# Optimization experiments

Measured on AMD Instinct MI355X. Metric: run time of the kernel, lower is better.

Reference implementation:

```python
import jax, jax.numpy as jnp
import numpy as np

H = 2048      # num_hidden
B = 2048      # batch_size
T = 64        # seq_length
C = 10        # num_classes


def setup_inputs() -> dict:
    key = jax.random.key(0)
    k = jax.random.split(key, 4)
    bound = float(np.sqrt(1.0 / H))  # uniform(-bound, bound) init as in the torch module
    return {
        "x": jax.random.normal(k[0], (B, T), dtype=jnp.float32),
        "W_hx": jax.random.uniform(k[1], (H, 1), jnp.float32, -bound, bound),
        "W_hh": jax.random.uniform(k[2], (H, H), jnp.float32, -bound, bound),
        "W_hy": jax.random.uniform(k[3], (H, C), jnp.float32, -bound, bound),
        "b_h": jnp.zeros((H, 1), jnp.float32),
        "b_p": jnp.zeros((C, 1), jnp.float32),
    }


def reference(x, W_hx, W_hh, W_hy, b_h, b_p):
    # x: [B, T]; hidden state kept as [H, B] to match the torch layout.
    xT = x.T  # [T, B] so scan iterates over time

    def step(h, xt):
        # W_hx @ x_t  : [H,1] @ [1,B] -> [H,B]; W_hh @ h : [H,B]
        h = jnp.tanh(W_hx @ xt[None, :] + W_hh @ h + b_h)
        return h, None

    h0 = jnp.zeros((W_hh.shape[0], x.shape[0]), x.dtype)
    hT, _ = jax.lax.scan(step, h0, xT)
    out = W_hy.T @ hT + b_p  # [C, B]
    return out.T             # [B, C]
```

## Files before the change

kernel.cpp:

```cpp
#include <hip/hip_runtime.h>
#include <cstdint>
#include <cstddef>
#include <cmath>

#define H  2048
#define BB 2048
#define TT 64
#define NC 10

typedef __bf16 bf16;
typedef bf16  bf16x8 __attribute__((ext_vector_type(8)));
typedef float f32x4  __attribute__((ext_vector_type(4)));

__device__ __forceinline__ void load_lds16(const void* g, void* l) {
    __builtin_amdgcn_global_load_lds(
        (__attribute__((address_space(1))) void*)(void*)g,
        (__attribute__((address_space(3))) void*)l,
        16, 0, 0);
}

__global__ void w_shuffle_kernel(const float* __restrict__ Whh,
                                 bf16* __restrict__ Wshuf) {
    int tid = blockIdx.x * blockDim.x + threadIdx.x;
    int sub = tid >> 6;
    int l   = tid & 63;
    int n16 = sub >> 6;
    int k32 = sub & 63;
    int n = n16 * 16 + (l & 15);
    int k = k32 * 32 + (l >> 4) * 8;
    const float* src = Whh + (size_t)n * H + k;
    bf16x8 o;
#pragma unroll
    for (int j = 0; j < 8; ++j) o[j] = (bf16)src[j];
    *(bf16x8*)(Wshuf + (size_t)tid * 8) = o;
}

__global__ void rnn_init(const float* __restrict__ x,
                         const float* __restrict__ Whx,
                         const float* __restrict__ bh,
                         bf16* __restrict__ S) {
    int b  = blockIdx.x;
    int i0 = threadIdx.x * 8;
    float xv = x[(size_t)b * TT];
    bf16x8 o;
#pragma unroll
    for (int j = 0; j < 8; ++j)
        o[j] = (bf16)tanhf(Whx[i0 + j] * xv + bh[i0 + j]);
    size_t sub  = (size_t)(b >> 4) * 64 + (i0 >> 5);
    size_t slot = (size_t)(b & 15) | (size_t)(((i0 >> 3) & 3) << 4);
    *(bf16x8*)(S + (sub * 64 + slot) * 8) = o;
}

#define PH_WAIT(NSTR) asm volatile("s_waitcnt vmcnt(" NSTR ")" ::: "memory")
#define SBAR0()       __builtin_amdgcn_sched_barrier(0)

__launch_bounds__(512)
__global__ void rnn_step(const float* __restrict__ x,
                         const float* __restrict__ Whx,
                         const float* __restrict__ bh,
                         const bf16*  __restrict__ Wshuf,
                         const bf16*  __restrict__ Sr,
                         bf16* __restrict__ Sw,
                         int t) {
    __shared__ __align__(16) char Ls[4][32768];

    const int tid  = threadIdx.x;
    const int w    = tid >> 6;
    const int lane = tid & 63;
    const int lrow = lane & 15;
    const int quad = lane >> 4;

    const int xcd = blockIdx.x & 7;
    const int loc = blockIdx.x >> 3;
    const int bm0 = (loc >> 1) * 128;
    const int bn0 = xcd * 256 + (loc & 1) * 128;

    const int qm   = w & 3;
    const int qn   = w >> 2;
    const int m16w = (bm0 >> 4) + qm * 2;
    const int cn0  = bn0 + qn * 64;

    const char* srcA = (const char*)Sr +
        ((size_t)((bm0 >> 4) + w) * 64) * 1024 + (size_t)lane * 16;
    const char* srcB = (const char*)Wshuf +
        ((size_t)((bn0 >> 4) + w) * 64) * 1024 + (size_t)lane * 16;

    f32x4 acc[2][4];
#pragma unroll
    for (int i = 0; i < 2; ++i)
#pragma unroll
        for (int j = 0; j < 4; ++j) acc[i][j] = (f32x4){0.f, 0.f, 0.f, 0.f};

#define ISSUE(RI, pp)                                                        \
    {                                                                        \
        _Pragma("unroll")                                                    \
        for (int j = 0; j < 2; ++j) {                                        \
            load_lds16(srcA + (size_t)(2 * (pp) + j) * 1024,                 \
                       &Ls[RI][(j * 16 + w) * 1024]);                        \
            load_lds16(srcB + (size_t)(2 * (pp) + j) * 1024,                 \
                       &Ls[RI][(j * 16 + 8 + w) * 1024]);                    \
        }                                                                    \
    }

#define COMPUTE(RI)                                                          \
    {                                                                        \
        _Pragma("unroll")                                                    \
        for (int j = 0; j < 2; ++j) {                                        \
            bf16x8 Af[2], Bf[4];                                             \
            _Pragma("unroll")                                                \
            for (int fm = 0; fm < 2; ++fm)                                   \
                Af[fm] = *(const bf16x8*)&Ls[RI]                             \
                    [(j * 16 + qm * 2 + fm) * 1024 + lane * 16];             \
            _Pragma("unroll")                                                \
            for (int fn = 0; fn < 4; ++fn)                                   \
                Bf[fn] = *(const bf16x8*)&Ls[RI]                             \
                    [(j * 16 + 8 + qn * 4 + fn) * 1024 + lane * 16];         \
            __builtin_amdgcn_s_setprio(1);                                   \
            _Pragma("unroll")                                                \
            for (int fm = 0; fm < 2; ++fm)                                   \
                _Pragma("unroll")                                            \
                for (int fn = 0; fn < 4; ++fn)                               \
                    acc[fm][fn] = __builtin_amdgcn_mfma_f32_16x16x32_bf16(   \
                        Af[fm], Bf[fn], acc[fm][fn], 0, 0, 0);               \
            __builtin_amdgcn_s_setprio(0);                                   \
        }                                                                    \
    }

#define PHASE(RI, RN, p, WNSTR, DOISS)                                       \
    {                                                                        \
        PH_WAIT(WNSTR);                                                      \
        SBAR0();                                                             \
        __builtin_amdgcn_s_barrier();                                        \
        SBAR0();                                                             \
        if (DOISS) ISSUE(RN, (p) + 3);                                       \
        SBAR0();                                                             \
        COMPUTE(RI);                                                         \
    }

    ISSUE(0, 0); SBAR0();
    ISSUE(1, 1); SBAR0();
    ISSUE(2, 2); SBAR0();

#pragma unroll 1
    for (int q = 0; q < 7; ++q) {
        int p = 4 * q;
        PHASE(0, 3, p + 0, "8", true);
        PHASE(1, 0, p + 1, "8", true);
        PHASE(2, 1, p + 2, "8", true);
        PHASE(3, 2, p + 3, "8", true);
    }
    PHASE(0, 3, 28, "8", true);
    PHASE(1, 0, 29, "8", false);
    PHASE(2, 1, 30, "4", false);
    PHASE(3, 2, 31, "0", false);

#undef PHASE
#undef COMPUTE
#undef ISSUE

    bf16* Lw = (bf16*)&Ls[0][0] + (size_t)w * 2048;
#pragma unroll
    for (int fm = 0; fm < 2; ++fm) {
        int rb = bm0 + qm * 32 + fm * 16 + quad * 4;
        float xv[4];
#pragma unroll
        for (int r = 0; r < 4; ++r) xv[r] = x[(size_t)(rb + r) * TT + t];
#pragma unroll
        for (int fn = 0; fn < 4; ++fn) {
            int col = cn0 + fn * 16 + lrow;
            float wx = Whx[col], bb = bh[col];
            int cbyte = (fn * 16 + lrow) * 2;
#pragma unroll
            for (int r = 0; r < 4; ++r) {
                int row_l = fm * 16 + quad * 4 + r;
                float z = acc[fm][fn][r] + wx * xv[r] + bb;
                *(bf16*)((char*)Lw + row_l * 128 +
                         (cbyte ^ ((row_l & 7) << 4))) = (bf16)tanhf(z);
            }
        }
    }
    __syncthreads();
#pragma unroll
    for (int fm = 0; fm < 2; ++fm) {
#pragma unroll
        for (int kc = 0; kc < 2; ++kc) {
            int row_l = fm * 16 + lrow;
            int cb    = (kc * 64 + quad * 16) ^ ((row_l & 7) << 4);
            bf16x8 v = *(const bf16x8*)((const char*)Lw + row_l * 128 + cb);
            size_t sub = (size_t)(m16w + fm) * 64 + (cn0 >> 5) + kc;
            *(bf16x8*)(Sw + (sub * 64 + lane) * 8) = v;
        }
    }
}

__global__ void out_proj(const bf16* __restrict__ S,
                         const float* __restrict__ Why,
                         const float* __restrict__ bp,
                         float* __restrict__ out) {
    int b = blockIdx.x, tid = threadIdx.x;
    int h0 = tid * 8;
    size_t sub  = (size_t)(b >> 4) * 64 + (h0 >> 5);
    size_t slot = (size_t)(b & 15) | (size_t)(((h0 >> 3) & 3) << 4);
    bf16x8 v = *(const bf16x8*)(S + (sub * 64 + slot) * 8);
    float p[NC];
#pragma unroll
    for (int c = 0; c < NC; ++c) p[c] = 0.f;
#pragma unroll
    for (int j = 0; j < 8; ++j) {
        float s = (float)v[j];
        const float* wr = Why + (size_t)(h0 + j) * NC;
#pragma unroll
        for (int c = 0; c < NC; ++c) p[c] += s * wr[c];
    }
    __shared__ float red[256 * NC];
#pragma unroll
    for (int c = 0; c < NC; ++c) red[tid * NC + c] = p[c];
    __syncthreads();
    for (int s = 128; s > 0; s >>= 1) {
        if (tid < s)
#pragma unroll
            for (int c = 0; c < NC; ++c) red[tid * NC + c] += red[(tid + s) * NC + c];
        __syncthreads();
    }
    if (tid < NC) out[(size_t)b * NC + tid] = red[tid] + bp[tid];
}

extern "C" void kernel_launch(void* const* d_in, const int* in_sizes, int n_in,
                              void* d_out, int out_size, void* d_ws, size_t ws_size,
                              hipStream_t stream) {
    const float* x   = (const float*)d_in[0];
    const float* Whx = (const float*)d_in[1];
    const float* Whh = (const float*)d_in[2];
    const float* Why = (const float*)d_in[3];
    const float* bh  = (const float*)d_in[4];
    const float* bp  = (const float*)d_in[5];
    float* out = (float*)d_out;

    bf16* Wshuf = (bf16*)d_ws;
    bf16* S0 = (bf16*)((char*)d_ws + (size_t)8 * 1024 * 1024);
    bf16* S1 = (bf16*)((char*)d_ws + (size_t)16 * 1024 * 1024);

    hipLaunchKernelGGL(w_shuffle_kernel, dim3((H * H / 8) / 256), dim3(256),
                       0, stream, Whh, Wshuf);

    hipLaunchKernelGGL(rnn_init, dim3(BB), dim3(256), 0, stream, x, Whx, bh, S1);

    for (int t = 1; t < TT; ++t) {
        const bf16* Srd = (t & 1) ? S1 : S0;
        bf16*       Swr = (t & 1) ? S0 : S1;
        hipLaunchKernelGGL(rnn_step, dim3(256), dim3(512), 0, stream,
                           x, Whx, bh, Wshuf, Srd, Swr, t);
    }

    hipLaunchKernelGGL(out_proj, dim3(BB), dim3(256), 0, stream, S0, Why, bp, out);
}
```

Before: 1.544 ms.

## Split K across wave halves with 64x64 warp tiles and LDS reduction

Each wave now computes a 64x64 output sub-tile over half of the K range instead of a 32x64 tile over the full K, so fragment loads feed more MFMAs (4x4 instead of 2x4 per k-slice). The two K-halves are combined through an LDS reduction before the tanh epilogue. This raises register use (16 accumulators) and adds an extra barrier and LDS traffic at the end of each step. Launch bounds now request 2 blocks per SM.

```diff
diff --git a/kernel.cpp b/kernel.cpp
--- a/kernel.cpp
+++ b/kernel.cpp
@@ -54,7 +54,7 @@
 #define PH_WAIT(NSTR) asm volatile("s_waitcnt vmcnt(" NSTR ")" ::: "memory")
 #define SBAR0()       __builtin_amdgcn_sched_barrier(0)
 
-__launch_bounds__(512)
+__launch_bounds__(512, 2)
 __global__ void rnn_step(const float* __restrict__ x,
                          const float* __restrict__ Whx,
                          const float* __restrict__ bh,
@@ -75,55 +75,51 @@
     const int bm0 = (loc >> 1) * 128;
     const int bn0 = xcd * 256 + (loc & 1) * 128;
 
-    const int qm   = w & 3;
-    const int qn   = w >> 2;
-    const int m16w = (bm0 >> 4) + qm * 2;
+    const int kh   = w >> 2;
+    const int s    = w & 3;
+    const int qm   = s & 1;
+    const int qn   = s >> 1;
     const int cn0  = bn0 + qn * 64;
+    const int kh16 = kh * 16;
 
     const char* srcA = (const char*)Sr +
         ((size_t)((bm0 >> 4) + w) * 64) * 1024 + (size_t)lane * 16;
     const char* srcB = (const char*)Wshuf +
         ((size_t)((bn0 >> 4) + w) * 64) * 1024 + (size_t)lane * 16;
 
-    f32x4 acc[2][4];
-#pragma unroll
-    for (int i = 0; i < 2; ++i)
+    f32x4 acc[4][4];
+#pragma unroll
+    for (int i = 0; i < 4; ++i)
 #pragma unroll
         for (int j = 0; j < 4; ++j) acc[i][j] = (f32x4){0.f, 0.f, 0.f, 0.f};
 
 #define ISSUE(RI, pp)                                                        \
     {                                                                        \
-        _Pragma("unroll")                                                    \
-        for (int j = 0; j < 2; ++j) {                                        \
-            load_lds16(srcA + (size_t)(2 * (pp) + j) * 1024,                 \
-                       &Ls[RI][(j * 16 + w) * 1024]);                        \
-            load_lds16(srcB + (size_t)(2 * (pp) + j) * 1024,                 \
-                       &Ls[RI][(j * 16 + 8 + w) * 1024]);                    \
-        }                                                                    \
+        load_lds16(srcA + (size_t)(pp) * 1024,        &Ls[RI][w * 1024]);    \
+        load_lds16(srcB + (size_t)(pp) * 1024,        &Ls[RI][(8 + w) * 1024]); \
+        load_lds16(srcA + (size_t)(32 + (pp)) * 1024, &Ls[RI][(16 + w) * 1024]); \
+        load_lds16(srcB + (size_t)(32 + (pp)) * 1024, &Ls[RI][(24 + w) * 1024]); \
     }
 
 #define COMPUTE(RI)                                                          \
     {                                                                        \
+        bf16x8 Af[4], Bf[4];                                                 \
         _Pragma("unroll")                                                    \
-        for (int j = 0; j < 2; ++j) {                                        \
-            bf16x8 Af[2], Bf[4];                                             \
-            _Pragma("unroll")                                                \
-            for (int fm = 0; fm < 2; ++fm)                                   \
-                Af[fm] = *(const bf16x8*)&Ls[RI]                             \
-                    [(j * 16 + qm * 2 + fm) * 1024 + lane * 16];             \
+        for (int fm = 0; fm < 4; ++fm)                                       \
+            Af[fm] = *(const bf16x8*)&Ls[RI]                                 \
+                [(kh16 + qm * 4 + fm) * 1024 + lane * 16];                   \
+        _Pragma("unroll")                                                    \
+        for (int fn = 0; fn < 4; ++fn)                                       \
+            Bf[fn] = *(const bf16x8*)&Ls[RI]                                 \
+                [(kh16 + 8 + qn * 4 + fn) * 1024 + lane * 16];               \
+        __builtin_amdgcn_s_setprio(1);                                       \
+        _Pragma("unroll")                                                    \
+        for (int fm = 0; fm < 4; ++fm)                                       \
             _Pragma("unroll")                                                \
             for (int fn = 0; fn < 4; ++fn)                                   \
-                Bf[fn] = *(const bf16x8*)&Ls[RI]                             \
-                    [(j * 16 + 8 + qn * 4 + fn) * 1024 + lane * 16];         \
-            __builtin_amdgcn_s_setprio(1);                                   \
-            _Pragma("unroll")                                                \
-            for (int fm = 0; fm < 2; ++fm)                                   \
-                _Pragma("unroll")                                            \
-                for (int fn = 0; fn < 4; ++fn)                               \
-                    acc[fm][fn] = __builtin_amdgcn_mfma_f32_16x16x32_bf16(   \
-                        Af[fm], Bf[fn], acc[fm][fn], 0, 0, 0);               \
-            __builtin_amdgcn_s_setprio(0);                                   \
-        }                                                                    \
+                acc[fm][fn] = __builtin_amdgcn_mfma_f32_16x16x32_bf16(       \
+                    Af[fm], Bf[fn], acc[fm][fn], 0, 0, 0);                   \
+        __builtin_amdgcn_s_setprio(0);                                       \
     }
 
 #define PHASE(RI, RN, p, WNSTR, DOISS)                                       \
@@ -158,10 +154,47 @@
 #undef COMPUTE
 #undef ISSUE
 
-    bf16* Lw = (bf16*)&Ls[0][0] + (size_t)w * 2048;
-#pragma unroll
-    for (int fm = 0; fm < 2; ++fm) {
-        int rb = bm0 + qm * 32 + fm * 16 + quad * 4;
+    {
+        char* red = &Ls[0][0];
+        const int pairbase = s * 16384;
+        if (kh == 0) {
+#pragma unroll
+            for (int fm = 2; fm < 4; ++fm)
+#pragma unroll
+                for (int fn = 0; fn < 4; ++fn)
+                    *(f32x4*)&red[pairbase + ((fm - 2) * 4 + fn) * 1024 +
+                                  lane * 16] = acc[fm][fn];
+        } else {
+#pragma unroll
+            for (int fm = 0; fm < 2; ++fm)
+#pragma unroll
+                for (int fn = 0; fn < 4; ++fn)
+                    *(f32x4*)&red[pairbase + 8192 + (fm * 4 + fn) * 1024 +
+                                  lane * 16] = acc[fm][fn];
+        }
+        __syncthreads();
+        if (kh == 0) {
+#pragma unroll
+            for (int fm = 0; fm < 2; ++fm)
+#pragma unroll
+                for (int fn = 0; fn < 4; ++fn)
+                    acc[fm][fn] += *(const f32x4*)&red[pairbase + 8192 +
+                        (fm * 4 + fn) * 1024 + lane * 16];
+        } else {
+#pragma unroll
+            for (int fm = 2; fm < 4; ++fm)
+#pragma unroll
+                for (int fn = 0; fn < 4; ++fn)
+                    acc[fm][fn] += *(const f32x4*)&red[pairbase +
+                        ((fm - 2) * 4 + fn) * 1024 + lane * 16];
+        }
+    }
+
+    bf16* Lw = (bf16*)&Ls[2][0] + (size_t)w * 2048;
+#pragma unroll
+    for (int fml = 0; fml < 2; ++fml) {
+        const int fm = kh * 2 + fml;
+        int rb = bm0 + qm * 64 + fm * 16 + quad * 4;
         float xv[4];
 #pragma unroll
         for (int r = 0; r < 4; ++r) xv[r] = x[(size_t)(rb + r) * TT + t];
@@ -172,22 +205,23 @@
             int cbyte = (fn * 16 + lrow) * 2;
 #pragma unroll
             for (int r = 0; r < 4; ++r) {
-                int row_l = fm * 16 + quad * 4 + r;
+                int row_l = fml * 16 + quad * 4 + r;
                 float z = acc[fm][fn][r] + wx * xv[r] + bb;
                 *(bf16*)((char*)Lw + row_l * 128 +
                          (cbyte ^ ((row_l & 7) << 4))) = (bf16)tanhf(z);
             }
         }
     }
-    __syncthreads();
-#pragma unroll
-    for (int fm = 0; fm < 2; ++fm) {
+#pragma unroll
+    for (int fml = 0; fml < 2; ++fml) {
+        const int fm = kh * 2 + fml;
 #pragma unroll
         for (int kc = 0; kc < 2; ++kc) {
-            int row_l = fm * 16 + lrow;
+            int row_l = fml * 16 + lrow;
             int cb    = (kc * 64 + quad * 16) ^ ((row_l & 7) << 4);
             bf16x8 v = *(const bf16x8*)((const char*)Lw + row_l * 128 + cb);
-            size_t sub = (size_t)(m16w + fm) * 64 + (cn0 >> 5) + kc;
+            size_t sub = (size_t)((bm0 >> 4) + qm * 4 + fm) * 64 +
+                         (cn0 >> 5) + kc;
             *(bf16x8*)(Sw + (sub * 64 + lane) * 8) = v;
         }
     }
```

Result: slower. 2.521 ms (+63.3%).
